# Optimization experiments

Hardware: AMD Instinct MI355X
Metric: run time of the kernel (lower is better)

The kernel has to match this reference:

```python
import jax, jax.numpy as jnp
import numpy as np
from jax import lax

GRID = 200      # _FIXED_GRID_LEN
SOFT_K = 50.0   # _SOFT_MASK_K
BN_EPS = 1e-5


def setup_inputs() -> dict:
    key = jax.random.key(0)
    ks = jax.random.split(key, 12)
    B, L = 8192, 2001
    f32 = jnp.float32
    inp = {
        'phase': jax.random.uniform(ks[0], (B, L), f32, -1.0, 1.0),
        'primary_flux': 0.01 * jax.random.normal(ks[1], (B, L), f32),
        'secondary_flux': 0.01 * jax.random.normal(ks[2], (B, L), f32),
        'odd_even_diff': 0.01 * jax.random.normal(ks[3], (B, L), f32),
        # TaylorGateLayerV8 params
        'A': jnp.asarray(0.01, f32),
        'Bp': jnp.asarray(1.0, f32),
        't0': jnp.asarray(0.0, f32),
        # BatchNorm1d(4), eval mode (running stats)
        'bn_gamma': jnp.ones((4,), f32),
        'bn_beta': jnp.zeros((4,), f32),
        'bn_mean': jnp.zeros((4,), f32),
        'bn_var': jnp.ones((4,), f32),
        # Conv1d(4,8,7) / Conv1d(8,16,5)
        'conv1_w': 0.1 * jax.random.normal(ks[4], (8, 4, 7), f32),
        'conv1_b': jnp.zeros((8,), f32),
        'conv2_w': 0.1 * jax.random.normal(ks[5], (16, 8, 5), f32),
        'conv2_b': jnp.zeros((16,), f32),
        # Linear(21, 1)
        'fc_w': 0.1 * jax.random.normal(ks[6], (1, 21), f32),
        'fc_b': jnp.zeros((1,), f32),
    }
    return inp


def _conv1d(x, w, b, pad):
    # x: (B, C, L), w: (O, C, K)
    y = lax.conv_general_dilated(x, w, window_strides=(1,), padding=[(pad, pad)],
                                 dimension_numbers=('NCH', 'OIH', 'NCH'))
    return y + b[None, :, None]


def _interp_linear_ac(x, out_len):
    # torch F.interpolate(mode='linear', align_corners=True) on (B, L) -> (B, out_len)
    L = x.shape[1]
    pos = jnp.linspace(0.0, L - 1.0, out_len)
    i0 = jnp.floor(pos).astype(jnp.int32)
    i1 = jnp.minimum(i0 + 1, L - 1)
    w = (pos - i0).astype(x.dtype)
    return x[:, i0] * (1.0 - w) + x[:, i1] * w


def reference(phase, primary_flux, secondary_flux, odd_even_diff,
              A, Bp, t0, bn_gamma, bn_beta, bn_mean, bn_var,
              conv1_w, conv1_b, conv2_w, conv2_b, fc_w, fc_b):
    # --- TaylorGateLayerV8: 2nd-order Taylor U-shape transit template ---
    gate = -A * jnp.clip(1.0 - Bp * (phase - t0) ** 2, 0.0, None)

    # --- CNN branch ---
    x = jnp.stack([gate, primary_flux, secondary_flux, odd_even_diff], axis=1)  # (B,4,L)
    inv = bn_gamma / jnp.sqrt(bn_var + BN_EPS)
    x = x * inv[None, :, None] + (bn_beta - bn_mean * inv)[None, :, None]
    x = jax.nn.relu(_conv1d(x, conv1_w, conv1_b, 3))
    x = jax.nn.relu(_conv1d(x, conv2_w, conv2_b, 2))
    cnn_out = jnp.mean(x, axis=2)  # AdaptiveAvgPool1d(1) -> (B,16)

    # --- shape features ---
    batch = primary_flux.shape[0]
    A_abs = jnp.abs(A) + 1e-8
    depth = jnp.clip(-primary_flux, 0.0, None)
    depth_norm = depth / A_abs
    depth_rs = _interp_linear_ac(depth, GRID)  # (B, 200)
    dx = 2.0 / (GRID - 1)                       # trapz over linspace(-1,1,200)
    auc_raw = dx * (jnp.sum(depth_rs, axis=1) - 0.5 * (depth_rs[:, 0] + depth_rs[:, -1]))
    auc_norm = auc_raw / A_abs
    dip_all = jax.nn.sigmoid(SOFT_K * (depth_norm - 0.1))
    flat_bot = jax.nn.sigmoid(SOFT_K * (depth_norm - 0.8))
    ingress = dip_all - flat_bot
    total = 1.0 - dip_all + ingress + flat_bot + 1e-8
    ingress = ingress / total
    flat_bot = flat_bot / total
    t14 = jnp.mean(ingress + flat_bot, axis=1) + 1e-8
    t12_t14 = jnp.mean(ingress, axis=1) / t14
    flat_bottom = jnp.mean(flat_bot, axis=1)
    B_bcast = jnp.broadcast_to(Bp, (batch,)).astype(depth.dtype)
    shape = jnp.stack([B_bcast, auc_raw, auc_norm, t12_t14, flat_bottom], axis=1)  # (B,5)

    features = jnp.concatenate([cnn_out, shape], axis=1)  # (B,21)
    logits = features @ fc_w.T + fc_b
    return jax.nn.sigmoid(logits)
```

## Files before the change

kernel.cpp:

```cpp
#include <hip/hip_runtime.h>
#include <math.h>

#define L_LEN 2001
#define CCH 224
#define NCH 9
#define XRECS 256
#define YRECS 240
#define NTB 15
#define NTC 14

typedef __attribute__((ext_vector_type(8))) short bf16x8;
typedef __attribute__((ext_vector_type(4))) float f32x4;
#if __has_builtin(__builtin_amdgcn_cvt_pk_bf16_f32)
typedef __attribute__((ext_vector_type(2))) __bf16 bf16x2_t;
#endif

union FragU { unsigned u[4]; uint2 u2[2]; uint4 u4; bf16x8 v; };

__device__ __forceinline__ unsigned short f2bf(float f) {
    unsigned u = __builtin_bit_cast(unsigned, f);
    u += 0x7fffu + ((u >> 16) & 1u);
    return (unsigned short)(u >> 16);
}
__device__ __forceinline__ unsigned bfpack(float lo, float hi) {
#if __has_builtin(__builtin_amdgcn_cvt_pk_bf16_f32)
    bf16x2_t r = __builtin_amdgcn_cvt_pk_bf16_f32(lo, hi);
    return __builtin_bit_cast(unsigned, r);
#else
    unsigned ul = __builtin_bit_cast(unsigned, lo);
    unsigned uh = __builtin_bit_cast(unsigned, hi);
    ul += 0x7fffu + ((ul >> 16) & 1u);
    uh += 0x7fffu + ((uh >> 16) & 1u);
    return __builtin_amdgcn_perm(uh, ul, 0x07060302);
#endif
}
__device__ __forceinline__ float fast_rcp(float x) { return __builtin_amdgcn_rcpf(x); }
__device__ __forceinline__ float fexp2(float x) {
#if __has_builtin(__builtin_amdgcn_exp2f)
    return __builtin_amdgcn_exp2f(x);
#else
    return __expf(x * 0.69314718f);
#endif
}

__global__ __launch_bounds__(256, 4)
void taylor_cnn_v9_wave(const float* __restrict__ phase, const float* __restrict__ primary,
                        const float* __restrict__ secondary, const float* __restrict__ oddeven,
                        const float* __restrict__ pA, const float* __restrict__ pBp,
                        const float* __restrict__ pT0,
                        const float* __restrict__ bng, const float* __restrict__ bnb,
                        const float* __restrict__ bnm, const float* __restrict__ bnv,
                        const float* __restrict__ w1, const float* __restrict__ b1,
                        const float* __restrict__ w2, const float* __restrict__ b2,
                        const float* __restrict__ fcw, const float* __restrict__ fcb,
                        float* __restrict__ out, int nrows)
{
    __shared__ __align__(16) unsigned int xs_i[4][XRECS * 2];
    __shared__ __align__(16) unsigned int y1_i[4][YRECS * 4];

    const int tid = threadIdx.x;
    const int l   = tid & 63;
    const int wid = tid >> 6;
    const int row = blockIdx.x * 4 + wid;
    if (row >= nrows) return;
    const long base = (long)row * L_LEN;

    unsigned int* xs = xs_i[wid];
    unsigned int* y1 = y1_i[wid];

    const int n    = l & 15;
    const int quad = l >> 4;

    const float A  = pA[0];
    const float Bp = pBp[0];
    const float t0 = pT0[0];
    const float A_abs = fabsf(A) + 1e-8f;
    const float rAabs = 1.0f / A_abs;
    const float nBp  = -Bp;
    const float cExp = -72.134766f * rAabs;

    float inv1, inv2, inv3, gInv0, off0, off1, off2, off3;
    {
        float iv0 = bng[0] / sqrtf(bnv[0] + 1e-5f);
        float iv1 = bng[1] / sqrtf(bnv[1] + 1e-5f);
        float iv2 = bng[2] / sqrtf(bnv[2] + 1e-5f);
        float iv3 = bng[3] / sqrtf(bnv[3] + 1e-5f);
        gInv0 = -A * iv0;
        inv1 = iv1; inv2 = iv2; inv3 = iv3;
        off0 = bnb[0] - bnm[0] * iv0;
        off1 = bnb[1] - bnm[1] * iv1;
        off2 = bnb[2] - bnm[2] * iv2;
        off3 = bnb[3] - bnm[3] * iv3;
    }

    bf16x8 a1;
#pragma unroll
    for (int jp = 0; jp < 8; ++jp) {
        int j = quad + 4 * (jp >> 2);
        int c = jp & 3;
        float v = (n < 8 && j < 7) ? w1[(n * 4 + c) * 7 + j] : 0.0f;
        a1[jp] = (short)f2bf(v);
    }
    bf16x8 a20, a21;
#pragma unroll
    for (int jp = 0; jp < 8; ++jp) {
        float v0 = w2[(n * 8 + jp) * 5 + quad];
        float v1 = (quad + 4 < 5) ? w2[(n * 8 + jp) * 5 + quad + 4] : 0.0f;
        a20[jp] = (short)f2bf(v0);
        a21[jp] = (short)f2bf(v1);
    }
    f32x4 cb1, cb2;
#pragma unroll
    for (int r = 0; r < 4; ++r) {
        cb1[r] = b1[(quad * 4 + r) & 7];
        cb2[r] = b2[quad * 4 + r];
    }
    float fw0 = fcw[quad * 4 + 0];
    float fw1 = fcw[quad * 4 + 1];
    float fw2 = fcw[quad * 4 + 2];
    float fw3 = fcw[quad * 4 + 3];

    float s_ing = 0.0f, s_fb = 0.0f;
    float m0 = 0.f, m1 = 0.f, m2 = 0.f, m3 = 0.f;

    float s_auc = 0.0f;
#pragma unroll
    for (int k = 0; k < 4; ++k) {
        int s = l + 64 * k;
        if (k < 3 || l < 8) {
            float pos = (float)s * (2000.0f / 199.0f);
            int i0 = (int)pos;
            if (i0 > 2000) i0 = 2000;
            int i1 = (i0 + 1 < L_LEN) ? i0 + 1 : 2000;
            float w  = pos - (float)i0;
            float d0 = fmaxf(-primary[base + i0], 0.f);
            float d1 = fmaxf(-primary[base + i1], 0.f);
            float v  = d0 * (1.0f - w) + d1 * w;
            float wt = (s == 0 || s == 199) ? 0.5f : 1.0f;
            s_auc += v * wt;
        }
    }

    auto aRec = [&](int m, int p, bool valid, bool core) {
        float ph = phase[base + p];
        float pf = primary[base + p];
        float sf = secondary[base + p];
        float oe = oddeven[base + p];
        float dd = ph - t0;
        float g  = fmaxf(fmaf(dd * dd, nBp, 1.0f), 0.0f);
        float x0 = fmaf(g,  gInv0, off0);
        float x1 = fmaf(pf, inv1, off1);
        float x2 = fmaf(sf, inv2, off2);
        float x3 = fmaf(oe, inv3, off3);
        unsigned d0 = bfpack(x0, x1);
        unsigned d1 = bfpack(x2, x3);
        if (!valid) { d0 = 0u; d1 = 0u; }
        *(uint2*)&xs[2 * m] = make_uint2(d0, d1);
        float depth = fmaxf(-pf, 0.0f);
        float e   = fexp2(depth * cExp);
        float dip = fast_rcp(fmaf(e, 148.413159f, 1.0f));
        float fb  = fast_rcp(fmaf(e, 2.35385267e17f, 1.0f));
        float ing = dip - fb;
        if (!core) { ing = 0.f; fb = 0.f; }
        s_ing += ing;
        s_fb  += fb;
    };

#pragma unroll 1
    for (int ch = 0; ch < NCH; ++ch) {
        const int c0 = ch * CCH;
        const int pb = c0 - 16;

        {
            bool v0  = (ch > 0) || (l >= 16);
            bool co0 = (l >= 16);
            int  p0  = pb + l;            if (p0 < 0) p0 = 0;
            int  p3  = pb + l + 192;
            bool v3  = (ch < NCH - 1) || (l < 33);
            bool co3 = v3 && (l < 48);
            if (p3 > 2000) p3 = 2000;
            aRec(l,        p0,           v0,   co0);
            aRec(l + 64,   pb + l + 64,  true, true);
            aRec(l + 128,  pb + l + 128, true, true);
            aRec(l + 192,  p3,           v3,   co3);
        }

        const bool bLo   = (ch == 0);
        const int  bFrom = (ch == NCH - 1) ? 13 : 99;
#pragma unroll 2
        for (int t = 0; t < NTB; ++t) {
            int qb = 16 * t + n + quad + 5;
            FragU bu;
            bu.u2[0] = *(const uint2*)&xs[2 * qb];
            bu.u2[1] = *(const uint2*)&xs[2 * (qb + 4)];
            f32x4 d = __builtin_amdgcn_mfma_f32_16x16x32_bf16(a1, bu.v, cb1, 0, 0, 0);
            if (l < 32) {
                int q = 16 * t + n;
                unsigned w0, w1_;
                if ((bLo && t == 0) || t >= bFrom) {
                    int p = c0 - 8 + q;
                    bool ok = ((unsigned)p < (unsigned)L_LEN);
                    w0  = ok ? bfpack(fmaxf(d[0], 0.f), fmaxf(d[1], 0.f)) : 0u;
                    w1_ = ok ? bfpack(fmaxf(d[2], 0.f), fmaxf(d[3], 0.f)) : 0u;
                } else {
                    w0  = bfpack(fmaxf(d[0], 0.f), fmaxf(d[1], 0.f));
                    w1_ = bfpack(fmaxf(d[2], 0.f), fmaxf(d[3], 0.f));
                }
                *(uint2*)&y1[4 * q + 2 * quad] = make_uint2(w0, w1_);
            }
        }

        const int maskT = (ch == NCH - 1) ? 13 : -1;
#pragma unroll 2
        for (int t = 0; t < NTC; ++t) {
            int q = 16 * t + n + quad + 6;
            FragU u0, u1;
            u0.u4 = *(const uint4*)&y1[4 * q];
            u1.u4 = *(const uint4*)&y1[4 * (q + 4)];
            f32x4 d = __builtin_amdgcn_mfma_f32_16x16x32_bf16(a20, u0.v, cb2, 0, 0, 0);
            d = __builtin_amdgcn_mfma_f32_16x16x32_bf16(a21, u1.v, d, 0, 0, 0);
            if (t == maskT) {
                float msk = (n == 0) ? 1.0f : 0.0f;
                m0 = fmaf(fmaxf(d[0], 0.f), msk, m0);
                m1 = fmaf(fmaxf(d[1], 0.f), msk, m1);
                m2 = fmaf(fmaxf(d[2], 0.f), msk, m2);
                m3 = fmaf(fmaxf(d[3], 0.f), msk, m3);
            } else {
                m0 += fmaxf(d[0], 0.f);
                m1 += fmaxf(d[1], 0.f);
                m2 += fmaxf(d[2], 0.f);
                m3 += fmaxf(d[3], 0.f);
            }
        }
    }

#pragma unroll
    for (int dlt = 8; dlt >= 1; dlt >>= 1) {
        m0 += __shfl_xor(m0, dlt);
        m1 += __shfl_xor(m1, dlt);
        m2 += __shfl_xor(m2, dlt);
        m3 += __shfl_xor(m3, dlt);
    }
    float part = m0 * fw0 + m1 * fw1 + m2 * fw2 + m3 * fw3;
    part = (n == 0) ? part : 0.0f;
    part += __shfl_xor(part, 16);
    part += __shfl_xor(part, 32);
#pragma unroll
    for (int dlt = 32; dlt >= 1; dlt >>= 1) {
        s_ing += __shfl_xor(s_ing, dlt);
        s_fb  += __shfl_xor(s_fb,  dlt);
        s_auc += __shfl_xor(s_auc, dlt);
    }

    if (l == 0) {
        float logit = fcb[0] + part * (1.0f / 2001.0f);
        float auc_raw  = (float)(2.0 / 199.0) * s_auc;
        float auc_norm = auc_raw / A_abs;
        float m_ing = s_ing / 2001.0f;
        float m_fb  = s_fb  / 2001.0f;
        float t14   = (s_ing + s_fb) / 2001.0f + 1e-8f;
        float t12   = m_ing / t14;

        logit += Bp       * fcw[16]
               + auc_raw  * fcw[17]
               + auc_norm * fcw[18]
               + t12      * fcw[19]
               + m_fb     * fcw[20];

        out[row] = 1.0f / (1.0f + expf(-logit));
    }
}

extern "C" void kernel_launch(void* const* d_in, const int* in_sizes, int n_in,
                              void* d_out, int out_size, void* d_ws, size_t ws_size,
                              hipStream_t stream) {
    const float* phase     = (const float*)d_in[0];
    const float* primary   = (const float*)d_in[1];
    const float* secondary = (const float*)d_in[2];
    const float* oddeven   = (const float*)d_in[3];
    const float* pA        = (const float*)d_in[4];
    const float* pBp       = (const float*)d_in[5];
    const float* pT0       = (const float*)d_in[6];
    const float* bng       = (const float*)d_in[7];
    const float* bnb       = (const float*)d_in[8];
    const float* bnm       = (const float*)d_in[9];
    const float* bnv       = (const float*)d_in[10];
    const float* w1        = (const float*)d_in[11];
    const float* b1        = (const float*)d_in[12];
    const float* w2        = (const float*)d_in[13];
    const float* b2        = (const float*)d_in[14];
    const float* fcw       = (const float*)d_in[15];
    const float* fcb       = (const float*)d_in[16];
    float* out = (float*)d_out;

    int nrows = in_sizes[0] / L_LEN;
    dim3 grid((nrows + 3) / 4), block(256);
    hipLaunchKernelGGL(taylor_cnn_v9_wave, grid, block, 0, stream,
                       phase, primary, secondary, oddeven, pA, pBp, pT0,
                       bng, bnb, bnm, bnv, w1, b1, w2, b2, fcw, fcb, out, nrows);
}
```

Baseline: 300.1 us.

## Use 32x32 MFMA for conv1 and vectorize per-lane input loads

Conv1 is restructured to use 32x32x16 bf16 MFMA instructions, two per 32-position tile, in place of fifteen 16x16x32 tiles. A single 16x16 tail tile covers the remaining positions. For non-final chunks, each lane now loads four consecutive floats per input with unaligned 128-bit loads and writes packed records with 128-bit LDS stores, instead of four strided scalar records. This is meant to cut MFMA issue count and the number of global and LDS instructions. The cost is more complex edge masking and extra weight and bias fragment registers.

```diff
diff --git a/kernel.cpp b/kernel.cpp
--- a/kernel.cpp
+++ b/kernel.cpp
@@ -6,11 +6,12 @@
 #define NCH 9
 #define XRECS 256
 #define YRECS 240
-#define NTB 15
 #define NTC 14
 
 typedef __attribute__((ext_vector_type(8))) short bf16x8;
 typedef __attribute__((ext_vector_type(4))) float f32x4;
+typedef __attribute__((ext_vector_type(16))) float f32x16;
+typedef __attribute__((ext_vector_type(4), aligned(4))) float f32x4u;
 #if __has_builtin(__builtin_amdgcn_cvt_pk_bf16_f32)
 typedef __attribute__((ext_vector_type(2))) __bf16 bf16x2_t;
 #endif
@@ -44,16 +45,16 @@
 }
 
 __global__ __launch_bounds__(256, 4)
-void taylor_cnn_v9_wave(const float* __restrict__ phase, const float* __restrict__ primary,
-                        const float* __restrict__ secondary, const float* __restrict__ oddeven,
-                        const float* __restrict__ pA, const float* __restrict__ pBp,
-                        const float* __restrict__ pT0,
-                        const float* __restrict__ bng, const float* __restrict__ bnb,
-                        const float* __restrict__ bnm, const float* __restrict__ bnv,
-                        const float* __restrict__ w1, const float* __restrict__ b1,
-                        const float* __restrict__ w2, const float* __restrict__ b2,
-                        const float* __restrict__ fcw, const float* __restrict__ fcb,
-                        float* __restrict__ out, int nrows)
+void taylor_cnn_v10_wave(const float* __restrict__ phase, const float* __restrict__ primary,
+                         const float* __restrict__ secondary, const float* __restrict__ oddeven,
+                         const float* __restrict__ pA, const float* __restrict__ pBp,
+                         const float* __restrict__ pT0,
+                         const float* __restrict__ bng, const float* __restrict__ bnb,
+                         const float* __restrict__ bnm, const float* __restrict__ bnv,
+                         const float* __restrict__ w1, const float* __restrict__ b1,
+                         const float* __restrict__ w2, const float* __restrict__ b2,
+                         const float* __restrict__ fcw, const float* __restrict__ fcb,
+                         float* __restrict__ out, int nrows)
 {
     __shared__ __align__(16) unsigned int xs_i[4][XRECS * 2];
     __shared__ __align__(16) unsigned int y1_i[4][YRECS * 4];
@@ -70,6 +71,8 @@
 
     const int n    = l & 15;
     const int quad = l >> 4;
+    const int c    = l & 31;
+    const int h    = l >> 5;
 
     const float A  = pA[0];
     const float Bp = pBp[0];
@@ -93,12 +96,28 @@
         off3 = bnb[3] - bnm[3] * iv3;
     }
 
+    bf16x8 a32_0, a32_1;
+#pragma unroll
+    for (int jp = 0; jp < 8; ++jp) {
+        int ch_  = jp & 3;
+        int tap0 = (jp >> 2) + 2 * h;
+        int tap1 = 4 + (jp >> 2) + 2 * h;
+        float v0 = (c < 8) ? w1[(c * 4 + ch_) * 7 + tap0] : 0.0f;
+        float v1 = (c < 8 && tap1 < 7) ? w1[(c * 4 + ch_) * 7 + tap1] : 0.0f;
+        a32_0[jp] = (short)f2bf(v0);
+        a32_1[jp] = (short)f2bf(v1);
+    }
+    f32x16 cb32;
+#pragma unroll
+    for (int r = 0; r < 16; ++r)
+        cb32[r] = (r < 4) ? b1[(r & 3) + 4 * h] : 0.0f;
+
     bf16x8 a1;
 #pragma unroll
     for (int jp = 0; jp < 8; ++jp) {
         int j = quad + 4 * (jp >> 2);
-        int c = jp & 3;
-        float v = (n < 8 && j < 7) ? w1[(n * 4 + c) * 7 + j] : 0.0f;
+        int cc = jp & 3;
+        float v = (n < 8 && j < 7) ? w1[(n * 4 + cc) * 7 + j] : 0.0f;
         a1[jp] = (short)f2bf(v);
     }
     bf16x8 a20, a21;
@@ -166,51 +185,104 @@
         s_fb  += fb;
     };
 
+    const float coreMask = (l >= 4 && l < 60) ? 1.0f : 0.0f;
+
 #pragma unroll 1
     for (int ch = 0; ch < NCH; ++ch) {
         const int c0 = ch * CCH;
         const int pb = c0 - 16;
-
-        {
-            bool v0  = (ch > 0) || (l >= 16);
+        const bool isFirst = (ch == 0);
+        const bool isLast  = (ch == NCH - 1);
+
+        if (!isLast) {
+            int p0 = pb + 4 * l;
+            bool zl = false;
+            if (isFirst && p0 < 0) { p0 = 0; zl = true; }
+            const f32x4u ph4 = *(const f32x4u*)&phase[base + p0];
+            const f32x4u pf4 = *(const f32x4u*)&primary[base + p0];
+            const f32x4u sf4 = *(const f32x4u*)&secondary[base + p0];
+            const f32x4u oe4 = *(const f32x4u*)&oddeven[base + p0];
+            unsigned dw[8];
+            float ingA = 0.f, fbA = 0.f;
+#pragma unroll
+            for (int j = 0; j < 4; ++j) {
+                float dd = ph4[j] - t0;
+                float g  = fmaxf(fmaf(dd * dd, nBp, 1.0f), 0.0f);
+                float x0 = fmaf(g,      gInv0, off0);
+                float x1 = fmaf(pf4[j], inv1,  off1);
+                float x2 = fmaf(sf4[j], inv2,  off2);
+                float x3 = fmaf(oe4[j], inv3,  off3);
+                dw[2 * j]     = bfpack(x0, x1);
+                dw[2 * j + 1] = bfpack(x2, x3);
+                float depth = fmaxf(-pf4[j], 0.0f);
+                float e   = fexp2(depth * cExp);
+                float dip = fast_rcp(fmaf(e, 148.413159f, 1.0f));
+                float fb  = fast_rcp(fmaf(e, 2.35385267e17f, 1.0f));
+                ingA += dip - fb;
+                fbA  += fb;
+            }
+            if (zl) {
+#pragma unroll
+                for (int j = 0; j < 8; ++j) dw[j] = 0u;
+            }
+            *(uint4*)&xs[8 * l]     = make_uint4(dw[0], dw[1], dw[2], dw[3]);
+            *(uint4*)&xs[8 * l + 4] = make_uint4(dw[4], dw[5], dw[6], dw[7]);
+            s_ing = fmaf(ingA, coreMask, s_ing);
+            s_fb  = fmaf(fbA,  coreMask, s_fb);
+        } else {
+            bool v0  = (l >= 16);
             bool co0 = (l >= 16);
-            int  p0  = pb + l;            if (p0 < 0) p0 = 0;
+            int  p0s = pb + l;
             int  p3  = pb + l + 192;
-            bool v3  = (ch < NCH - 1) || (l < 33);
+            bool v3  = (l < 33);
             bool co3 = v3 && (l < 48);
             if (p3 > 2000) p3 = 2000;
-            aRec(l,        p0,           v0,   co0);
+            aRec(l,        p0s,          true, co0); (void)v0;
             aRec(l + 64,   pb + l + 64,  true, true);
             aRec(l + 128,  pb + l + 128, true, true);
             aRec(l + 192,  p3,           v3,   co3);
         }
 
-        const bool bLo   = (ch == 0);
-        const int  bFrom = (ch == NCH - 1) ? 13 : 99;
+        {
+            const int cb = c + 2 * h + 5;
 #pragma unroll 2
-        for (int t = 0; t < NTB; ++t) {
-            int qb = 16 * t + n + quad + 5;
-            FragU bu;
-            bu.u2[0] = *(const uint2*)&xs[2 * qb];
-            bu.u2[1] = *(const uint2*)&xs[2 * (qb + 4)];
-            f32x4 d = __builtin_amdgcn_mfma_f32_16x16x32_bf16(a1, bu.v, cb1, 0, 0, 0);
-            if (l < 32) {
-                int q = 16 * t + n;
-                unsigned w0, w1_;
-                if ((bLo && t == 0) || t >= bFrom) {
-                    int p = c0 - 8 + q;
-                    bool ok = ((unsigned)p < (unsigned)L_LEN);
-                    w0  = ok ? bfpack(fmaxf(d[0], 0.f), fmaxf(d[1], 0.f)) : 0u;
-                    w1_ = ok ? bfpack(fmaxf(d[2], 0.f), fmaxf(d[3], 0.f)) : 0u;
-                } else {
-                    w0  = bfpack(fmaxf(d[0], 0.f), fmaxf(d[1], 0.f));
-                    w1_ = bfpack(fmaxf(d[2], 0.f), fmaxf(d[3], 0.f));
+            for (int T = 0; T < 7; ++T) {
+                const int R0 = 32 * T + cb;
+                FragU b0, b1f;
+                b0.u2[0]  = *(const uint2*)&xs[2 * R0];
+                b0.u2[1]  = *(const uint2*)&xs[2 * R0 + 2];
+                b1f.u2[0] = *(const uint2*)&xs[2 * R0 + 8];
+                b1f.u2[1] = *(const uint2*)&xs[2 * R0 + 10];
+                f32x16 d = __builtin_amdgcn_mfma_f32_32x32x16_bf16(a32_0, b0.v,  cb32, 0, 0, 0);
+                d        = __builtin_amdgcn_mfma_f32_32x32x16_bf16(a32_1, b1f.v, d,    0, 0, 0);
+                unsigned w0  = bfpack(fmaxf(d[0], 0.f), fmaxf(d[1], 0.f));
+                unsigned w1_ = bfpack(fmaxf(d[2], 0.f), fmaxf(d[3], 0.f));
+                if (isFirst && T == 0) {
+                    if (c < 8) { w0 = 0u; w1_ = 0u; }
                 }
-                *(uint2*)&y1[4 * q + 2 * quad] = make_uint2(w0, w1_);
+                if (isLast && T == 6) {
+                    if (c > 24) { w0 = 0u; w1_ = 0u; }
+                }
+                *(uint2*)&y1[4 * (32 * T + c) + 2 * h] = make_uint2(w0, w1_);
+            }
+            if (!isLast) {
+                int qb = 224 + n + quad + 5;
+                FragU bu;
+                bu.u2[0] = *(const uint2*)&xs[2 * qb];
+                bu.u2[1] = *(const uint2*)&xs[2 * (qb + 4)];
+                f32x4 d = __builtin_amdgcn_mfma_f32_16x16x32_bf16(a1, bu.v, cb1, 0, 0, 0);
+                if (l < 32) {
+                    unsigned w0  = bfpack(fmaxf(d[0], 0.f), fmaxf(d[1], 0.f));
+                    unsigned w1_ = bfpack(fmaxf(d[2], 0.f), fmaxf(d[3], 0.f));
+                    *(uint2*)&y1[4 * (224 + n) + 2 * quad] = make_uint2(w0, w1_);
+                }
+            } else {
+                if (l < 32)
+                    *(uint2*)&y1[4 * (224 + n) + 2 * quad] = make_uint2(0u, 0u);
             }
         }
 
-        const int maskT = (ch == NCH - 1) ? 13 : -1;
+        const int maskT = isLast ? 13 : -1;
 #pragma unroll 2
         for (int t = 0; t < NTC; ++t) {
             int q = 16 * t + n + quad + 6;
@@ -295,7 +367,7 @@
 
     int nrows = in_sizes[0] / L_LEN;
     dim3 grid((nrows + 3) / 4), block(256);
-    hipLaunchKernelGGL(taylor_cnn_v9_wave, grid, block, 0, stream,
+    hipLaunchKernelGGL(taylor_cnn_v10_wave, grid, block, 0, stream,
                        phase, primary, secondary, oddeven, pA, pBp, pT0,
                        bng, bnb, bnm, bnv, w1, b1, w2, b2, fcw, fcb, out, nrows);
 }
```

Result: faster. 291.2 us (-3.0%).
